# Performance work log

Measured on AMD Instinct MI355X. Metric: run time of the kernel, lower is better.

Reference implementation:

```python
import jax, jax.numpy as jnp
import numpy as np


def setup_inputs() -> dict:
    key = jax.random.key(0)
    k1, k2, k3 = jax.random.split(key, 3)
    B, Q, K, D = 4, 2048, 2048, 1024
    query = jax.random.normal(k1, (B, Q, D), dtype=jnp.float32)
    value = jax.random.normal(k2, (B, K, D), dtype=jnp.float32)
    attention_mask = jax.random.randint(k3, (B, Q, K), 0, 2, dtype=jnp.int32)
    return {"query": query, "value": value, "attention_mask": attention_mask}


def reference(query, value, attention_mask):
    # key defaults to value in the original module
    D = query.shape[-1]
    # scores[b,q,k] = sum_d (query[b,q,d] + key[b,k,d])
    #              = rowsum(query)[b,q] + rowsum(key)[b,k]  (separable outer-sum,
    # avoids the (B,Q,K,D) intermediate the torch code materializes)
    q_sum = query.sum(-1)                    # (B, Q)
    k_sum = value.sum(-1)                    # (B, K)  (key == value)
    scores = q_sum[:, :, None] + k_sum[:, None, :]   # (B, Q, K)
    scores = scores / jnp.sqrt(jnp.asarray(D, scores.dtype))  # use_scale=True
    mask_value = -1e9
    scores = scores + (1.0 - attention_mask.astype(scores.dtype)) * mask_value
    attention_weights = jax.nn.softmax(scores, axis=-1)       # (B, Q, K)
    context_vector = jnp.einsum('bqk,bkd->bqd', attention_weights, value)
    return (context_vector, attention_weights)
```

## Files before the change

### kernel.cpp

```cpp
#include <hip/hip_runtime.h>
#include <stdint.h>

#define BB 4
#define QQ 2048
#define KK 2048
#define DD 1024

__device__ inline unsigned short f2bf(float f) {
    unsigned int u = __float_as_uint(f);
    unsigned int r = (u + 0x7fffu + ((u >> 16) & 1u)) >> 16;
    return (unsigned short)r;
}

typedef short bf16x8 __attribute__((ext_vector_type(8)));
typedef float f32x4  __attribute__((ext_vector_type(4)));

__device__ inline void async16(const void* g, void* l) {
    __builtin_amdgcn_global_load_lds(
        (const __attribute__((address_space(1))) unsigned int*)g,
        (__attribute__((address_space(3))) unsigned int*)l,
        16, 0, 0);
}

__global__ __launch_bounds__(256) void transpose_conv(const float* __restrict__ V,
                                                      unsigned short* __restrict__ Vt) {
    int bid = blockIdx.x;
    int b  = bid >> 9;
    int r  = bid & 511;
    int kt = r >> 4;
    int dt = r & 15;
    int k0 = kt * 64, d0 = dt * 64;
    __shared__ float tile[64 * 65];
    int t = threadIdx.x;
    for (int i = 0; i < 4; i++) {
        int idx = i * 256 + t;
        int row = idx >> 4;
        int c4  = idx & 15;
        float4 v = *(const float4*)(V + (size_t)(b * KK + k0 + row) * DD + d0 + c4 * 4);
        float* p = &tile[row * 65 + c4 * 4];
        p[0] = v.x; p[1] = v.y; p[2] = v.z; p[3] = v.w;
    }
    __syncthreads();
    for (int i = 0; i < 4; i++) {
        int idx = i * 256 + t;
        int dr = idx >> 4;
        int kc = idx & 15;
        ushort4 o;
        o.x = f2bf(tile[(kc * 4 + 0) * 65 + dr]);
        o.y = f2bf(tile[(kc * 4 + 1) * 65 + dr]);
        o.z = f2bf(tile[(kc * 4 + 2) * 65 + dr]);
        o.w = f2bf(tile[(kc * 4 + 3) * 65 + dr]);
        *(ushort4*)(Vt + (size_t)(b * DD + d0 + dr) * KK + k0 + kc * 4) = o;
    }
}

__global__ __launch_bounds__(256) void rowexp(const float* __restrict__ V,
                                              float* __restrict__ e) {
    int wave = threadIdx.x >> 6, lane = threadIdx.x & 63;
    int row = blockIdx.x * 4 + wave;
    const float* p = V + (size_t)row * DD;
    float s = 0.f;
    for (int j = 0; j < 4; j++) {
        float4 v = *(const float4*)(p + j * 256 + lane * 4);
        s += v.x + v.y + v.z + v.w;
    }
    for (int off = 32; off; off >>= 1) s += __shfl_xor(s, off, 64);
    if (lane == 0) e[row] = __expf(s * 0.03125f);
}

__global__ __launch_bounds__(256) void weights_k(const int* __restrict__ mask,
                                                 const float* __restrict__ e,
                                                 float* __restrict__ wout,
                                                 unsigned short* __restrict__ wb16) {
    int wave = threadIdx.x >> 6, lane = threadIdx.x & 63;
    int row = blockIdx.x * 4 + wave;
    int b = row >> 11;
    const int4*   mp = (const int4*)(mask + (size_t)row * KK);
    const float4* ep = (const float4*)(e + (size_t)b * KK);
    float4 w[8];
    float s = 0.f;
    for (int j = 0; j < 8; j++) {
        int4   m  = mp[lane + j * 64];
        float4 ev = ep[lane + j * 64];
        w[j].x = m.x ? ev.x : 0.f;
        w[j].y = m.y ? ev.y : 0.f;
        w[j].z = m.z ? ev.z : 0.f;
        w[j].w = m.w ? ev.w : 0.f;
        s += (w[j].x + w[j].y) + (w[j].z + w[j].w);
    }
    for (int off = 32; off; off >>= 1) s += __shfl_xor(s, off, 64);
    float rS = 1.f / s;
    float4*  wp = (float4*)(wout + (size_t)row * KK);
    ushort4* bp = (ushort4*)(wb16 + (size_t)row * KK);
    for (int j = 0; j < 8; j++) {
        float4 v = w[j];
        v.x *= rS; v.y *= rS; v.z *= rS; v.w *= rS;
        wp[lane + j * 64] = v;
        ushort4 pk;
        pk.x = f2bf(v.x); pk.y = f2bf(v.y); pk.z = f2bf(v.z); pk.w = f2bf(v.w);
        bp[lane + j * 64] = pk;
    }
}

__global__ __launch_bounds__(256) void gemm_ctx(const unsigned short* __restrict__ Wb,
                                                const unsigned short* __restrict__ Vt,
                                                float* __restrict__ ctx) {
    int bid = blockIdx.x;
    int b  = bid >> 7;
    int r  = bid & 127;
    int qt = r >> 3, dt = r & 7;
    int q0 = qt * 128, n0 = dt * 128;
    __shared__ unsigned short As[128 * 64];
    __shared__ unsigned short Bs[128 * 64];
    int tid = threadIdx.x, wave = tid >> 6, lane = tid & 63;
    int quad = lane >> 4, lm = lane & 15;
    int wm = wave >> 1, wn = wave & 1;

    int srow   = lane >> 3;
    int schunk = (lane & 7) ^ srow;
    const unsigned short* Ag = Wb + (size_t)(b * QQ + q0 + wave * 8 + srow) * KK + schunk * 8;
    const unsigned short* Bg = Vt + (size_t)(b * DD + n0 + wave * 8 + srow) * KK + schunk * 8;
    unsigned short* lA = &As[(wave * 8) * 64];
    unsigned short* lB = &Bs[(wave * 8) * 64];

    int m7 = lm & 7;
    int xa0 = lm * 64 + ((0 + quad) ^ m7) * 8;
    int xa1 = lm * 64 + ((4 + quad) ^ m7) * 8;

    f32x4 acc[4][4];
    for (int i = 0; i < 4; i++)
        for (int j = 0; j < 4; j++) acc[i][j] = 0.f;

    for (int k0 = 0; k0 < KK; k0 += 64) {
        if (k0) __syncthreads();
        for (int c = 0; c < 4; c++) {
            async16(Ag + (size_t)(c * 32) * KK + k0, lA + c * 32 * 64);
            async16(Bg + (size_t)(c * 32) * KK + k0, lB + c * 32 * 64);
        }
        __syncthreads();
        bf16x8 a[4][2], bv[4][2];
        for (int i = 0; i < 4; i++) {
            a[i][0]  = *(const bf16x8*)&As[(wm * 64 + i * 16) * 64 + xa0];
            a[i][1]  = *(const bf16x8*)&As[(wm * 64 + i * 16) * 64 + xa1];
            bv[i][0] = *(const bf16x8*)&Bs[(wn * 64 + i * 16) * 64 + xa0];
            bv[i][1] = *(const bf16x8*)&Bs[(wn * 64 + i * 16) * 64 + xa1];
        }
        for (int h = 0; h < 2; h++)
            for (int i = 0; i < 4; i++)
                for (int j = 0; j < 4; j++)
                    acc[i][j] = __builtin_amdgcn_mfma_f32_16x16x32_bf16(a[i][h], bv[j][h], acc[i][j], 0, 0, 0);
    }
    for (int i = 0; i < 4; i++) {
        int rowb = q0 + wm * 64 + i * 16 + quad * 4;
        for (int j = 0; j < 4; j++) {
            int col = n0 + wn * 64 + j * 16 + lm;
            for (int rr = 0; rr < 4; rr++)
                ctx[(size_t)(b * QQ + rowb + rr) * DD + col] = acc[i][j][rr];
        }
    }
}

extern "C" void kernel_launch(void* const* d_in, const int* in_sizes, int n_in,
                              void* d_out, int out_size, void* d_ws, size_t ws_size,
                              hipStream_t stream) {
    const float* value = (const float*)d_in[1];
    const int*   mask  = (const int*)d_in[2];
    float* out = (float*)d_out;

    unsigned short* Vt = (unsigned short*)d_ws;
    unsigned short* Wb = Vt + (size_t)BB * DD * KK;
    float* e = (float*)(Wb + (size_t)BB * QQ * KK);

    float* ctx  = out;
    float* wout = out + (size_t)BB * QQ * DD;

    rowexp<<<(BB * KK) / 4, 256, 0, stream>>>(value, e);
    transpose_conv<<<BB * 512, 256, 0, stream>>>(value, Vt);
    weights_k<<<(BB * QQ) / 4, 256, 0, stream>>>(mask, e, wout, Wb);
    gemm_ctx<<<BB * 128, 256, 0, stream>>>(Wb, Vt, ctx);
}
```

Baseline: 246.5 us.

## Double-buffer GEMM LDS tiles with 256x128 block tiles and reordered grid

Rewrites the context GEMM to use 256x128 output tiles with a K step of 32 and two LDS buffers, so the async global-to-LDS loads for the next K slice overlap the MFMAs on the current one and one barrier per iteration is removed. The block index now puts the d-tile in the high bits, so blocks sharing the same weight rows and V tiles run close together for L2 reuse. The grid shrinks to 256 blocks, which is about one per CU, and launch bounds are set to one block per CU. Each wave holds more accumulators (32 MFMA tiles), raising register pressure and leaving fewer waves to hide latency. The transpose and rowexp launches are also swapped.

Measured after the change: 295.1 us. 1.2x slower.

```diff
diff --git a/kernel.cpp b/kernel.cpp
--- a/kernel.cpp
+++ b/kernel.cpp
@@ -102,56 +102,61 @@
     }
 }
 
-__global__ __launch_bounds__(256) void gemm_ctx(const unsigned short* __restrict__ Wb,
-                                                const unsigned short* __restrict__ Vt,
-                                                float* __restrict__ ctx) {
+__global__ __launch_bounds__(256, 1) void gemm_ctx(const unsigned short* __restrict__ Wb,
+                                                   const unsigned short* __restrict__ Vt,
+                                                   float* __restrict__ ctx) {
     int bid = blockIdx.x;
-    int b  = bid >> 7;
-    int r  = bid & 127;
-    int qt = r >> 3, dt = r & 7;
-    int q0 = qt * 128, n0 = dt * 128;
-    __shared__ unsigned short As[128 * 64];
-    __shared__ unsigned short Bs[128 * 64];
+    int g  = bid & 31;
+    int dt = bid >> 5;
+    int b  = g >> 3, qt = g & 7;
+    int q0 = qt * 256, n0 = dt * 128;
+    __shared__ unsigned short As[2][256 * 32];
+    __shared__ unsigned short Bs[2][128 * 32];
     int tid = threadIdx.x, wave = tid >> 6, lane = tid & 63;
     int quad = lane >> 4, lm = lane & 15;
     int wm = wave >> 1, wn = wave & 1;
 
-    int srow   = lane >> 3;
-    int schunk = (lane & 7) ^ srow;
-    const unsigned short* Ag = Wb + (size_t)(b * QQ + q0 + wave * 8 + srow) * KK + schunk * 8;
-    const unsigned short* Bg = Vt + (size_t)(b * DD + n0 + wave * 8 + srow) * KK + schunk * 8;
-    unsigned short* lA = &As[(wave * 8) * 64];
-    unsigned short* lB = &Bs[(wave * 8) * 64];
+    int srow   = lane >> 2;
+    int schunk = (lane & 3) ^ (srow & 3);
+    const unsigned short* Ag = Wb + (size_t)(b * QQ + q0 + wave * 16 + srow) * KK + schunk * 8;
+    const unsigned short* Bg = Vt + (size_t)(b * DD + n0 + wave * 16 + srow) * KK + schunk * 8;
 
-    int m7 = lm & 7;
-    int xa0 = lm * 64 + ((0 + quad) ^ m7) * 8;
-    int xa1 = lm * 64 + ((4 + quad) ^ m7) * 8;
+    int x4 = lm & 3;
+    int aoff = lm * 32 + (quad ^ x4) * 8;
 
-    f32x4 acc[4][4];
-    for (int i = 0; i < 4; i++)
+    f32x4 acc[8][4];
+    for (int i = 0; i < 8; i++)
         for (int j = 0; j < 4; j++) acc[i][j] = 0.f;
 
-    for (int k0 = 0; k0 < KK; k0 += 64) {
-        if (k0) __syncthreads();
-        for (int c = 0; c < 4; c++) {
-            async16(Ag + (size_t)(c * 32) * KK + k0, lA + c * 32 * 64);
-            async16(Bg + (size_t)(c * 32) * KK + k0, lB + c * 32 * 64);
+    {
+        unsigned short* lA = &As[0][(wave * 16) * 32];
+        unsigned short* lB = &Bs[0][(wave * 16) * 32];
+        for (int c = 0; c < 4; c++) async16(Ag + (size_t)(c * 64) * KK, lA + c * 64 * 32);
+        for (int c = 0; c < 2; c++) async16(Bg + (size_t)(c * 64) * KK, lB + c * 64 * 32);
+    }
+
+    for (int it = 0; it < 64; it++) {
+        __syncthreads();
+        if (it + 1 < 64) {
+            int k0 = (it + 1) * 32;
+            unsigned short* lA = &As[(it + 1) & 1][(wave * 16) * 32];
+            unsigned short* lB = &Bs[(it + 1) & 1][(wave * 16) * 32];
+            for (int c = 0; c < 4; c++) async16(Ag + (size_t)(c * 64) * KK + k0, lA + c * 64 * 32);
+            for (int c = 0; c < 2; c++) async16(Bg + (size_t)(c * 64) * KK + k0, lB + c * 64 * 32);
         }
-        __syncthreads();
-        bf16x8 a[4][2], bv[4][2];
-        for (int i = 0; i < 4; i++) {
-            a[i][0]  = *(const bf16x8*)&As[(wm * 64 + i * 16) * 64 + xa0];
-            a[i][1]  = *(const bf16x8*)&As[(wm * 64 + i * 16) * 64 + xa1];
-            bv[i][0] = *(const bf16x8*)&Bs[(wn * 64 + i * 16) * 64 + xa0];
-            bv[i][1] = *(const bf16x8*)&Bs[(wn * 64 + i * 16) * 64 + xa1];
-        }
-        for (int h = 0; h < 2; h++)
-            for (int i = 0; i < 4; i++)
-                for (int j = 0; j < 4; j++)
-                    acc[i][j] = __builtin_amdgcn_mfma_f32_16x16x32_bf16(a[i][h], bv[j][h], acc[i][j], 0, 0, 0);
+        const unsigned short* A = As[it & 1];
+        const unsigned short* B = Bs[it & 1];
+        bf16x8 a[8], bv[4];
+        for (int j = 0; j < 4; j++)
+            bv[j] = *(const bf16x8*)&B[(wn * 64 + j * 16) * 32 + aoff];
+        for (int i = 0; i < 8; i++)
+            a[i]  = *(const bf16x8*)&A[(wm * 128 + i * 16) * 32 + aoff];
+        for (int i = 0; i < 8; i++)
+            for (int j = 0; j < 4; j++)
+                acc[i][j] = __builtin_amdgcn_mfma_f32_16x16x32_bf16(a[i], bv[j], acc[i][j], 0, 0, 0);
     }
-    for (int i = 0; i < 4; i++) {
-        int rowb = q0 + wm * 64 + i * 16 + quad * 4;
+    for (int i = 0; i < 8; i++) {
+        int rowb = q0 + wm * 128 + i * 16 + quad * 4;
         for (int j = 0; j < 4; j++) {
             int col = n0 + wn * 64 + j * 16 + lm;
             for (int rr = 0; rr < 4; rr++)
@@ -174,8 +179,8 @@
     float* ctx  = out;
     float* wout = out + (size_t)BB * QQ * DD;
 
+    transpose_conv<<<BB * 512, 256, 0, stream>>>(value, Vt);
     rowexp<<<(BB * KK) / 4, 256, 0, stream>>>(value, e);
-    transpose_conv<<<BB * 512, 256, 0, stream>>>(value, Vt);
     weights_k<<<(BB * QQ) / 4, 256, 0, stream>>>(mask, e, wout, Wb);
-    gemm_ctx<<<BB * 128, 256, 0, stream>>>(Wb, Vt, ctx);
+    gemm_ctx<<<BB * 64, 256, 0, stream>>>(Wb, Vt, ctx);
 }
```
